# Kernel tuning notes

Measured on AMD Instinct MI355X. Metric: run time of the kernel, lower is better.

Reference implementation:

```python
import jax, jax.numpy as jnp
import numpy as np

N_QUBIT = 14
N_LAYER = 16
BATCH = 512
DIM = 2 ** N_QUBIT

# wire 0 is the most-significant bit (deepquantum convention: state.reshape([2]*n), wire i = axis i)
_bits = (np.arange(DIM)[:, None] >> (N_QUBIT - 1 - np.arange(N_QUBIT))) & 1
SIGNS = jnp.asarray(2.0 * _bits - 1.0, dtype=jnp.float32)  # (DIM, n_qubit), -1 for bit=0, +1 for bit=1


def _apply_1q(state, gate, w):
    # state: (B, DIM) complex64; gate: (2,2) complex
    B = state.shape[0]
    left, right = 2 ** w, 2 ** (N_QUBIT - w - 1)
    st = state.reshape(B, left, 2, right)
    return jnp.einsum('ab,xlbr->xlar', gate, st).reshape(B, DIM)


def _cnot(state, c, t):
    # CNOT control c, target t: X on target where control bit = 1
    B = state.shape[0]
    st = state.reshape((B,) + (2,) * N_QUBIT)
    ax_c, ax_t = c + 1, t + 1
    a0 = jnp.take(st, 0, axis=ax_c)
    a1 = jnp.take(st, 1, axis=ax_c)
    a1 = jnp.flip(a1, axis=ax_t if ax_t < ax_c else ax_t - 1)  # flip size-2 axis == X gate
    return jnp.stack([a0, a1], axis=ax_c).reshape(B, DIM)


def _rz_layer(state, thetas):
    # RZ(th) = diag(e^{-i th/2}, e^{+i th/2}) on every wire -> single fused diagonal phase
    return state * jnp.exp(0.5j * (SIGNS @ thetas))


def _ry_layer(state, thetas):
    for w in range(N_QUBIT):
        c = jnp.cos(thetas[w] * 0.5)
        s = jnp.sin(thetas[w] * 0.5)
        gate = jnp.stack([jnp.stack([c, -s]), jnp.stack([s, c])]).astype(jnp.complex64)
        state = _apply_1q(state, gate, w)
    return state


def _circuit(z, theta):
    state = z.reshape(z.shape[0], DIM)
    for l in range(N_LAYER):
        state = _rz_layer(state, theta[l, 0])
        state = _ry_layer(state, theta[l, 1])
        state = _rz_layer(state, theta[l, 2])
        for w in range(N_QUBIT):  # cnot_ring
            state = _cnot(state, w, (w + 1) % N_QUBIT)
    return state


def _split(state, w):
    B = state.shape[0]
    st = state.reshape(B, 2 ** w, 2, 2 ** (N_QUBIT - w - 1))
    return st[:, :, 0, :], st[:, :, 1, :]


def _expectations(state):
    outs = []
    for w in (0, 1):  # <Z_w> = sum |psi_0|^2 - |psi_1|^2
        p0, p1 = _split(state, w)
        outs.append(jnp.sum(jnp.abs(p0) ** 2 - jnp.abs(p1) ** 2, axis=(1, 2)))
    cross0 = None
    for w in (0, 1):  # <X_w> = 2 Re sum conj(psi_0) psi_1
        p0, p1 = _split(state, w)
        cr = jnp.conj(p0) * p1
        if w == 0:
            cross0 = cr
        outs.append(2.0 * jnp.sum(jnp.real(cr), axis=(1, 2)))
    outs.append(2.0 * jnp.sum(jnp.imag(cross0), axis=(1, 2)))  # <Y_0> = 2 Im sum conj(psi_0) psi_1
    return jnp.stack(outs, axis=1).astype(jnp.float32)  # (B, 5)


def setup_inputs() -> dict:
    key = jax.random.key(0)
    k1, k2, k3, k4 = jax.random.split(key, 4)
    zr = jax.random.normal(k1, (BATCH, DIM), dtype=jnp.float32)
    zi = jax.random.normal(k2, (BATCH, DIM), dtype=jnp.float32)
    z = (zr + 1j * zi).astype(jnp.complex64)
    z = z / jnp.linalg.norm(z, axis=1, keepdims=True)  # normalized quantum states
    z = z[:, :, None]  # (B, 2^n, 1) per docstring
    theta = jax.random.normal(k3, (N_LAYER, 3, N_QUBIT), dtype=jnp.float32)
    y = jax.random.randint(k4, (BATCH,), 0, 5)
    return {"z": z, "theta": theta, "y": y}


def reference(z, theta, y):
    state = _circuit(z, theta)
    output = _expectations(state)
    logp = jax.nn.log_softmax(output, axis=1)
    loss = -jnp.mean(jnp.take_along_axis(logp, y[:, None], axis=1))
    return (loss, output)
```

## Files before the change

kernel.cpp:

```cpp
#include <hip/hip_runtime.h>
#include <hip/hip_bf16.h>

#define NQ     14
#define DIM    16384
#define NLAYER 16
#define BATCH  512
#define NT     1024

typedef float v2f __attribute__((ext_vector_type(2)));

__device__ __forceinline__ constexpr int POSB(int x){ return (x ^ ((x >> 5) & 31)) << 3; }

__device__ __forceinline__ float bf2f(unsigned int u16){
  union { unsigned int i; float f; } v; v.i = u16 << 16; return v.f;
}

__device__ __forceinline__ float thv(const void* th, int i, bool b16){
  return b16 ? bf2f(((const unsigned short*)th)[i]) : ((const float*)th)[i];
}

__device__ int srcF(int x){
  int v = x;
  #pragma unroll
  for (int k = 13; k >= 0; --k){
    int tb = 13 - ((k + 1) % 14);
    v ^= ((v >> (13 - k)) & 1) << tb;
  }
  return v;
}

__device__ __forceinline__ v2f cmul(v2f a, v2f b){
  v2f t, d;
  asm("v_pk_mul_f32 %0, %1, %2 op_sel:[0,0] op_sel_hi:[1,0]"
      : "=v"(t) : "v"(a), "v"(b));
  asm("v_pk_fma_f32 %0, %1, %2, %3 op_sel:[1,1,0] op_sel_hi:[0,1,1] neg_lo:[0,1,0]"
      : "=v"(d) : "v"(a), "v"(b), "v"(t));
  return d;
}

__device__ __forceinline__ void rot2(v2f& a0, v2f& a1, float c, float s){
  v2f c2 = (v2f){c, c}, s2 = (v2f){s, s};
  v2f t0 = a0;
  a0 = a0 * c2 - a1 * s2;
  a1 = t0 * s2 + a1 * c2;
}

template<int CTRL>
__device__ __forceinline__ v2f quad_swap(v2f a){
  union { float f; int i; } xl, xh;
  xl.f = a.x; xh.f = a.y;
  union { int i; float f; } rl, rh;
  rl.i = __builtin_amdgcn_mov_dpp(xl.i, CTRL, 0xf, 0xf, true);
  rh.i = __builtin_amdgcn_mov_dpp(xh.i, CTRL, 0xf, 0xf, true);
  return (v2f){rl.f, rh.f};
}

__global__ __launch_bounds__(NT) __attribute__((amdgpu_waves_per_eu(4, 4)))
void qnn_circuit(const void* __restrict__ zraw,
                 const void* __restrict__ theta,
                 float* __restrict__ out)
{
  __shared__ v2f   S[DIM];
  __shared__ v2f   ph0H[128], ph0L[128], ph2Ht[128], ph2Lt[128];
  __shared__ float csT[28];
  __shared__ int   sHB[128], sLB[128];
  __shared__ float red[16*5];

  char* Sb = (char*)S;
  const int t = threadIdx.x;
  const int b = blockIdx.x;

  int pred = 0;
  if (t < 336){
    unsigned int w  = ((const unsigned int*)theta)[t];
    unsigned int lo = w & 0xffffu;
    unsigned int e  = (lo >> 7) & 0xffu;
    pred = (e >= 100 && e <= 140) || (lo == 0);
  }
  const bool th_b16 = (__syncthreads_count(pred) > 250);

  pred = 0;
  if (t < 256){
    unsigned int w  = ((const unsigned int*)zraw)[t];
    unsigned int lo = w & 0xffffu;
    unsigned int e  = (lo >> 7) & 0xffu;
    pred = (e >= 88 && e <= 140) || (lo == 0);
  }
  const bool z_b16 = (__syncthreads_count(pred) > 160);

  if (t < 128){ sHB[t] = POSB(srcF(t << 7)); sLB[t] = POSB(srcF(t)); }

  if (z_b16){
    const uint4* zb = (const uint4*)((const unsigned short*)zraw + (size_t)b * (DIM * 2));
    #pragma unroll 1
    for (int jj = 0; jj < 4; ++jj){
      int x4 = t + NT * jj;
      uint4 w = zb[x4];
      int xb = x4 * 4;
      *(v2f*)(Sb + POSB(xb+0)) = (v2f){bf2f(w.x & 0xffffu), bf2f(w.x >> 16)};
      *(v2f*)(Sb + POSB(xb+1)) = (v2f){bf2f(w.y & 0xffffu), bf2f(w.y >> 16)};
      *(v2f*)(Sb + POSB(xb+2)) = (v2f){bf2f(w.z & 0xffffu), bf2f(w.z >> 16)};
      *(v2f*)(Sb + POSB(xb+3)) = (v2f){bf2f(w.w & 0xffffu), bf2f(w.w >> 16)};
    }
  } else {
    const float4* zf = (const float4*)((const float*)zraw + (size_t)b * DIM);
    #pragma unroll 1
    for (int jj = 0; jj < 4; ++jj){
      int x4 = t + NT * jj;
      float4 w = zf[x4];
      int xb = x4 * 4;
      *(v2f*)(Sb + POSB(xb+0)) = (v2f){w.x, 0.f};
      *(v2f*)(Sb + POSB(xb+1)) = (v2f){w.y, 0.f};
      *(v2f*)(Sb + POSB(xb+2)) = (v2f){w.z, 0.f};
      *(v2f*)(Sb + POSB(xb+3)) = (v2f){w.w, 0.f};
    }
  }
  __syncthreads();

  const int pwb = POSB(t);
  const int hb  = t >> 7;
  const int slB = sLB[t & 127];

  const int wv  = t >> 6, L = t & 63;
  const int pbA  = POSB((wv << 10) | L);
  const int pbB1 = POSB((wv << 10) | ((L >> 2) << 6) | (L & 3));
  const int hB1  = (wv << 3) | (L >> 3);
  const int lB1  = L & 7;
  const float sg0 = (t & 1) ? 1.f : -1.f;
  const float sg1 = (t & 2) ? 1.f : -1.f;

  for (int l = 0; l < NLAYER; ++l){
    const int thb = l * 42;

    if (t < 512){
      int grp = t >> 7, idx = t & 127;
      int tz = thb + ((grp >= 2) ? 28 : 0);
      float ph = 0.f;
      if ((grp & 1) == 0){
        #pragma unroll
        for (int w = 0; w < 7; ++w)
          ph += (((idx >> (6 - w)) & 1) ? 0.5f : -0.5f) * thv(theta, tz + w, th_b16);
      } else {
        #pragma unroll
        for (int w = 7; w < 14; ++w)
          ph += (((idx >> (13 - w)) & 1) ? 0.5f : -0.5f) * thv(theta, tz + w, th_b16);
      }
      float sn, cs; sincosf(ph, &sn, &cs);
      v2f v = (v2f){cs, sn};
      if      (grp == 0) ph0H[idx] = v;
      else if (grp == 1) ph0L[idx] = v;
      else if (grp == 2) ph2Ht[idx] = v;
      else               ph2Lt[(idx & 3) | (((idx >> 6) & 1) << 2) | (((idx >> 2) & 15) << 3)] = v;
    } else if (t < 512 + 14){
      int q = t - 512;
      float sn, cs; sincosf(0.5f * thv(theta, thb + 14 + q, th_b16), &sn, &cs);
      csT[2*q] = cs; csT[2*q+1] = sn;
    }

    {
      v2f g[16];
      if (l == 0){
        #pragma unroll
        for (int j = 0; j < 16; ++j) g[j] = *(v2f*)(Sb + (pwb ^ (j << 13)));
      } else {
        #pragma unroll
        for (int j = 0; j < 16; ++j)
          g[j] = *(v2f*)(Sb + (sHB[hb + 8*j] ^ slB));
      }
      __syncthreads();

      {
        v2f cl = ph0L[t & 127];
        #pragma unroll
        for (int j = 0; j < 16; ++j)
          g[j] = cmul(g[j], cmul(ph0H[hb + 8*j], cl));
      }
      #pragma unroll
      for (int q = 0; q < 4; ++q){
        float c = csT[2*q], sn = csT[2*q+1];
        int m = 8 >> q;
        #pragma unroll
        for (int j = 0; j < 16; ++j){
          if (j & m) continue;
          rot2(g[j], g[j | m], c, sn);
        }
      }
      #pragma unroll
      for (int j = 0; j < 16; ++j) *(v2f*)(Sb + (pwb ^ (j << 13))) = g[j];
    }
    __syncthreads();

    {
      v2f h[16];
      #pragma unroll
      for (int j = 0; j < 16; ++j) h[j] = *(v2f*)(Sb + (pbA ^ ((j << 9) | (j << 4))));
      #pragma unroll
      for (int q = 0; q < 4; ++q){
        float c = csT[2*(4+q)], sn = csT[2*(4+q)+1];
        int m = 8 >> q;
        #pragma unroll
        for (int j = 0; j < 16; ++j){
          if (j & m) continue;
          rot2(h[j], h[j | m], c, sn);
        }
      }
      {
        float c13 = csT[26], s13 = csT[27];
        v2f c13v = (v2f){c13, c13};
        v2f s13v = (v2f){sg0 * s13, sg0 * s13};
        #pragma unroll
        for (int j = 0; j < 16; ++j){
          v2f p = quad_swap<0xB1>(h[j]);
          h[j] = h[j] * c13v + p * s13v;
        }
        float c12 = csT[24], s12 = csT[25];
        v2f c12v = (v2f){c12, c12};
        v2f s12v = (v2f){sg1 * s12, sg1 * s12};
        #pragma unroll
        for (int j = 0; j < 16; ++j){
          v2f p = quad_swap<0x4E>(h[j]);
          h[j] = h[j] * c12v + p * s12v;
        }
      }
      #pragma unroll
      for (int j = 0; j < 16; ++j) *(v2f*)(Sb + (pbA ^ ((j << 9) | (j << 4)))) = h[j];
    }
    __threadfence_block();

    {
      v2f h[16];
      #pragma unroll
      for (int j = 0; j < 16; ++j)
        h[j] = *(v2f*)(Sb + (pbB1 ^ ((j << 5) ^ ((j >> 3) << 3))));
      #pragma unroll
      for (int q = 0; q < 4; ++q){
        float c = csT[2*(8+q)], sn = csT[2*(8+q)+1];
        int m = 8 >> q;
        #pragma unroll
        for (int j = 0; j < 16; ++j){
          if (j & m) continue;
          rot2(h[j], h[j | m], c, sn);
        }
      }
      {
        v2f chh = ph2Ht[hB1];
        #pragma unroll
        for (int j = 0; j < 16; ++j)
          h[j] = cmul(h[j], cmul(chh, ph2Lt[lB1 | (j << 3)]));
      }
      #pragma unroll
      for (int j = 0; j < 16; ++j)
        *(v2f*)(Sb + (pbB1 ^ ((j << 5) ^ ((j >> 3) << 3)))) = h[j];
    }
    __syncthreads();
  }

  float z0=0.f, z1=0.f, x0s=0.f, x1s=0.f, y0s=0.f;
  {
    v2f g[16];
    #pragma unroll
    for (int j = 0; j < 16; ++j)
      g[j] = *(v2f*)(Sb + (sHB[hb + 8*j] ^ slB));

    #pragma unroll
    for (int j = 0; j < 16; ++j){
      float pw = g[j].x*g[j].x + g[j].y*g[j].y;
      z0 += (j & 8) ? -pw : pw;
      z1 += (j & 4) ? -pw : pw;
    }
    #pragma unroll
    for (int j = 0; j < 8; ++j){
      v2f p0 = g[j], p1 = g[j+8];
      x0s += 2.f*(p0.x*p1.x + p0.y*p1.y);
      y0s += 2.f*(p0.x*p1.y - p0.y*p1.x);
    }
    #pragma unroll
    for (int j = 0; j < 16; ++j){
      if (j & 4) continue;
      v2f p0 = g[j], p1 = g[j|4];
      x1s += 2.f*(p0.x*p1.x + p0.y*p1.y);
    }
  }
  #pragma unroll
  for (int o = 32; o >= 1; o >>= 1){
    z0  += __shfl_down(z0,  o, 64);
    z1  += __shfl_down(z1,  o, 64);
    x0s += __shfl_down(x0s, o, 64);
    x1s += __shfl_down(x1s, o, 64);
    y0s += __shfl_down(y0s, o, 64);
  }
  int wid = t >> 6, lane = t & 63;
  if (lane == 0){
    red[wid*5+0]=z0; red[wid*5+1]=z1; red[wid*5+2]=x0s; red[wid*5+3]=x1s; red[wid*5+4]=y0s;
  }
  __syncthreads();
  if (t < 5){
    float sum = 0.f;
    #pragma unroll
    for (int w = 0; w < 16; ++w) sum += red[w*5 + t];
    out[1 + b*5 + t] = sum;
  }
}

__global__ __launch_bounds__(512)
void qnn_loss(const int* __restrict__ y, float* __restrict__ out)
{
  __shared__ float red[8];
  int t = threadIdx.x;
  const float* o = out + 1 + t*5;
  float o0=o[0], o1=o[1], o2=o[2], o3=o[3], o4=o[4];
  float m = fmaxf(fmaxf(fmaxf(o0,o1), fmaxf(o2,o3)), o4);
  float sum = expf(o0-m)+expf(o1-m)+expf(o2-m)+expf(o3-m)+expf(o4-m);
  float lse = m + logf(sum);
  int yi = y[t]; yi = yi < 0 ? 0 : (yi > 4 ? 4 : yi);
  float lb = lse - o[yi];

  #pragma unroll
  for (int ofs = 32; ofs >= 1; ofs >>= 1) lb += __shfl_down(lb, ofs, 64);
  if ((t & 63) == 0) red[t >> 6] = lb;
  __syncthreads();
  if (t == 0){
    float s = 0.f;
    #pragma unroll
    for (int w = 0; w < 8; ++w) s += red[w];
    out[0] = s / (float)BATCH;
  }
}

extern "C" void kernel_launch(void* const* d_in, const int* in_sizes, int n_in,
                              void* d_out, int out_size, void* d_ws, size_t ws_size,
                              hipStream_t stream)
{
  const void* z     = d_in[0];
  const void* theta = d_in[1];
  const int*  y     = (const int*)d_in[2];
  float*      out   = (float*)d_out;

  qnn_circuit<<<BATCH, NT, 0, stream>>>(z, theta, out);
  qnn_loss<<<1, 512, 0, stream>>>(y, out);
}
```

Baseline: 253.3 us.

## Precompute per-layer phase and rotation tables in a separate kernel via workspace

Adds a small pre-kernel that computes the per-layer RZ phase tables and RY cos/sin values once into the workspace. The main circuit kernel then only copies these from global memory each layer, instead of every block redoing sincos and theta decoding. The sHB index lookups are also hoisted into wave-uniform registers via readfirstlane. The cost is an extra kernel launch, plus a fallback path that is used when the workspace is too small.

```diff
diff --git a/kernel.cpp b/kernel.cpp
--- a/kernel.cpp
+++ b/kernel.cpp
@@ -6,6 +6,10 @@
 #define NLAYER 16
 #define BATCH  512
 #define NT     1024
+
+#define TBL_V2F_STRIDE   528
+#define TBL_F_STRIDE     1056
+#define TBL_BYTES        (NLAYER * TBL_V2F_STRIDE * 8)
 
 typedef float v2f __attribute__((ext_vector_type(2)));
 
@@ -55,21 +59,14 @@
   return (v2f){rl.f, rh.f};
 }
 
-__global__ __launch_bounds__(NT) __attribute__((amdgpu_waves_per_eu(4, 4)))
-void qnn_circuit(const void* __restrict__ zraw,
-                 const void* __restrict__ theta,
-                 float* __restrict__ out)
+__device__ __forceinline__ int ph2lt_pos(int idx){
+  return (idx & 3) | (((idx >> 6) & 1) << 2) | (((idx >> 2) & 15) << 3);
+}
+
+__global__ __launch_bounds__(512)
+void qnn_tables(const void* __restrict__ theta, float* __restrict__ ws)
 {
-  __shared__ v2f   S[DIM];
-  __shared__ v2f   ph0H[128], ph0L[128], ph2Ht[128], ph2Lt[128];
-  __shared__ float csT[28];
-  __shared__ int   sHB[128], sLB[128];
-  __shared__ float red[16*5];
-
-  char* Sb = (char*)S;
-  const int t = threadIdx.x;
-  const int b = blockIdx.x;
-
+  const int t = threadIdx.x, l = blockIdx.x;
   int pred = 0;
   if (t < 336){
     unsigned int w  = ((const unsigned int*)theta)[t];
@@ -78,8 +75,62 @@
     pred = (e >= 100 && e <= 140) || (lo == 0);
   }
   const bool th_b16 = (__syncthreads_count(pred) > 250);
-
-  pred = 0;
+  const int thb = l * 42;
+
+  {
+    int grp = t >> 7, idx = t & 127;
+    int tz = thb + ((grp >= 2) ? 28 : 0);
+    float ph = 0.f;
+    if ((grp & 1) == 0){
+      #pragma unroll
+      for (int w = 0; w < 7; ++w)
+        ph += (((idx >> (6 - w)) & 1) ? 0.5f : -0.5f) * thv(theta, tz + w, th_b16);
+    } else {
+      #pragma unroll
+      for (int w = 7; w < 14; ++w)
+        ph += (((idx >> (13 - w)) & 1) ? 0.5f : -0.5f) * thv(theta, tz + w, th_b16);
+    }
+    float sn, cs; sincosf(ph, &sn, &cs);
+    int pos = (grp < 3) ? ((grp << 7) | idx) : (384 | ph2lt_pos(idx));
+    ((v2f*)ws)[l * TBL_V2F_STRIDE + pos] = (v2f){cs, sn};
+  }
+  if (t < 14){
+    float sn, cs; sincosf(0.5f * thv(theta, thb + 14 + t, th_b16), &sn, &cs);
+    ws[l * TBL_F_STRIDE + 1024 + 2*t]     = cs;
+    ws[l * TBL_F_STRIDE + 1024 + 2*t + 1] = sn;
+  }
+}
+
+template<int USE_WS>
+__global__ __launch_bounds__(NT) __attribute__((amdgpu_waves_per_eu(4, 4)))
+void qnn_circuit(const void* __restrict__ zraw,
+                 const void* __restrict__ theta,
+                 float* __restrict__ out,
+                 const float* __restrict__ ws)
+{
+  __shared__ v2f   S[DIM];
+  __shared__ v2f   tbl[512];
+  __shared__ float csT[28];
+  __shared__ int   sHB[128], sLB[128];
+  __shared__ float red[16*5];
+
+  char* Sb = (char*)S;
+  const int t = threadIdx.x;
+  const int b = blockIdx.x;
+
+  bool th_b16 = false;
+  if constexpr (!USE_WS){
+    int predt = 0;
+    if (t < 336){
+      unsigned int w  = ((const unsigned int*)theta)[t];
+      unsigned int lo = w & 0xffffu;
+      unsigned int e  = (lo >> 7) & 0xffu;
+      predt = (e >= 100 && e <= 140) || (lo == 0);
+    }
+    th_b16 = (__syncthreads_count(predt) > 250);
+  }
+
+  int pred = 0;
   if (t < 256){
     unsigned int w  = ((const unsigned int*)zraw)[t];
     unsigned int lo = w & 0xffffu;
@@ -121,40 +172,48 @@
   const int hb  = t >> 7;
   const int slB = sLB[t & 127];
 
+  int sH[16];
+  #pragma unroll
+  for (int j = 0; j < 16; ++j)
+    sH[j] = __builtin_amdgcn_readfirstlane(sHB[hb + 8*j]);
+
   const int wv  = t >> 6, L = t & 63;
   const int pbA  = POSB((wv << 10) | L);
   const int pbB1 = POSB((wv << 10) | ((L >> 2) << 6) | (L & 3));
-  const int hB1  = (wv << 3) | (L >> 3);
-  const int lB1  = L & 7;
+  const int hB1  = 256 | (wv << 3) | (L >> 3);
+  const int lB1  = 384 | (L & 7);
   const float sg0 = (t & 1) ? 1.f : -1.f;
   const float sg1 = (t & 2) ? 1.f : -1.f;
 
   for (int l = 0; l < NLAYER; ++l){
-    const int thb = l * 42;
-
-    if (t < 512){
-      int grp = t >> 7, idx = t & 127;
-      int tz = thb + ((grp >= 2) ? 28 : 0);
-      float ph = 0.f;
-      if ((grp & 1) == 0){
-        #pragma unroll
-        for (int w = 0; w < 7; ++w)
-          ph += (((idx >> (6 - w)) & 1) ? 0.5f : -0.5f) * thv(theta, tz + w, th_b16);
-      } else {
-        #pragma unroll
-        for (int w = 7; w < 14; ++w)
-          ph += (((idx >> (13 - w)) & 1) ? 0.5f : -0.5f) * thv(theta, tz + w, th_b16);
-      }
-      float sn, cs; sincosf(ph, &sn, &cs);
-      v2f v = (v2f){cs, sn};
-      if      (grp == 0) ph0H[idx] = v;
-      else if (grp == 1) ph0L[idx] = v;
-      else if (grp == 2) ph2Ht[idx] = v;
-      else               ph2Lt[(idx & 3) | (((idx >> 6) & 1) << 2) | (((idx >> 2) & 15) << 3)] = v;
-    } else if (t < 512 + 14){
-      int q = t - 512;
-      float sn, cs; sincosf(0.5f * thv(theta, thb + 14 + q, th_b16), &sn, &cs);
-      csT[2*q] = cs; csT[2*q+1] = sn;
+    if constexpr (USE_WS){
+      if (t < 512)
+        tbl[t] = ((const v2f*)ws)[l * TBL_V2F_STRIDE + t];
+      else if (t < 512 + 28)
+        csT[t - 512] = ws[l * TBL_F_STRIDE + 1024 + (t - 512)];
+    } else {
+      const int thb = l * 42;
+      if (t < 512){
+        int grp = t >> 7, idx = t & 127;
+        int tz = thb + ((grp >= 2) ? 28 : 0);
+        float ph = 0.f;
+        if ((grp & 1) == 0){
+          #pragma unroll
+          for (int w = 0; w < 7; ++w)
+            ph += (((idx >> (6 - w)) & 1) ? 0.5f : -0.5f) * thv(theta, tz + w, th_b16);
+        } else {
+          #pragma unroll
+          for (int w = 7; w < 14; ++w)
+            ph += (((idx >> (13 - w)) & 1) ? 0.5f : -0.5f) * thv(theta, tz + w, th_b16);
+        }
+        float sn, cs; sincosf(ph, &sn, &cs);
+        int pos = (grp < 3) ? ((grp << 7) | idx) : (384 | ph2lt_pos(idx));
+        tbl[pos] = (v2f){cs, sn};
+      } else if (t < 512 + 14){
+        int q = t - 512;
+        float sn, cs; sincosf(0.5f * thv(theta, thb + 14 + q, th_b16), &sn, &cs);
+        csT[2*q] = cs; csT[2*q+1] = sn;
+      }
     }
 
     {
@@ -165,15 +224,15 @@
       } else {
         #pragma unroll
         for (int j = 0; j < 16; ++j)
-          g[j] = *(v2f*)(Sb + (sHB[hb + 8*j] ^ slB));
+          g[j] = *(v2f*)(Sb + (sH[j] ^ slB));
       }
       __syncthreads();
 
       {
-        v2f cl = ph0L[t & 127];
+        v2f cl = tbl[128 | (t & 127)];
         #pragma unroll
         for (int j = 0; j < 16; ++j)
-          g[j] = cmul(g[j], cmul(ph0H[hb + 8*j], cl));
+          g[j] = cmul(g[j], cmul(tbl[hb + 8*j], cl));
       }
       #pragma unroll
       for (int q = 0; q < 4; ++q){
@@ -243,10 +302,10 @@
         }
       }
       {
-        v2f chh = ph2Ht[hB1];
+        v2f chh = tbl[hB1];
         #pragma unroll
         for (int j = 0; j < 16; ++j)
-          h[j] = cmul(h[j], cmul(chh, ph2Lt[lB1 | (j << 3)]));
+          h[j] = cmul(h[j], cmul(chh, tbl[lB1 | (j << 3)]));
       }
       #pragma unroll
       for (int j = 0; j < 16; ++j)
@@ -260,7 +319,7 @@
     v2f g[16];
     #pragma unroll
     for (int j = 0; j < 16; ++j)
-      g[j] = *(v2f*)(Sb + (sHB[hb + 8*j] ^ slB));
+      g[j] = *(v2f*)(Sb + (sH[j] ^ slB));
 
     #pragma unroll
     for (int j = 0; j < 16; ++j){
@@ -335,7 +394,13 @@
   const void* theta = d_in[1];
   const int*  y     = (const int*)d_in[2];
   float*      out   = (float*)d_out;
-
-  qnn_circuit<<<BATCH, NT, 0, stream>>>(z, theta, out);
+  float*      ws    = (float*)d_ws;
+
+  if (ws_size >= (size_t)TBL_BYTES){
+    qnn_tables<<<NLAYER, 512, 0, stream>>>(theta, ws);
+    qnn_circuit<1><<<BATCH, NT, 0, stream>>>(z, theta, out, ws);
+  } else {
+    qnn_circuit<0><<<BATCH, NT, 0, stream>>>(z, theta, out, ws);
+  }
   qnn_loss<<<1, 512, 0, stream>>>(y, out);
 }
```

Measured after the change: 249.0 us, median of 2. Within noise of the previous version (-1.7%).
